# Kernel tuning notes

Measured on AMD Instinct MI355X. Metric: run time of the kernel, lower is better.

The kernel has to match this reference:

```python
import jax, jax.numpy as jnp
import numpy as np
from jax import lax

ALPHA = 2.0          # HausdorffDistanceLoss alpha
W_CE, W_BD, W_HD = 1.0, 0.5, 0.5   # combined-loss weights
NOSEED = 1e4         # sentinel 1D distance for lines with no seed pixel (>> max real distance)


def _sq_dt_binary(seed):
    """Exact squared 1D distance (along last axis) to nearest True pixel. seed: [..., L] bool."""
    L = seed.shape[-1]
    idx = jnp.arange(L, dtype=jnp.int32)
    left = lax.cummax(jnp.where(seed, idx, -1), axis=seed.ndim - 1)
    right = lax.cummin(jnp.where(seed, idx, 2 * L), axis=seed.ndim - 1, reverse=True)
    dl = jnp.where(left >= 0, (idx - left).astype(jnp.float32), jnp.float32(NOSEED))
    dr = jnp.where(right < 2 * L, (right - idx).astype(jnp.float32), jnp.float32(NOSEED))
    d = jnp.minimum(dl, dr)
    return d * d


def _sq_dt_general(f):
    """d[j] = min_y f[..., y] + (j - y)^2 along last axis (lower envelope, brute force via scan)."""
    L = f.shape[-1]
    idx = jnp.arange(L, dtype=f.dtype)
    fm = jnp.moveaxis(f, -1, 0)  # [L, ...]
    def step(carry, inp):
        fy, y = inp
        cand = fy[..., None] + (idx - y) ** 2  # [..., L]
        return jnp.minimum(carry, cand), None
    init = jnp.full(f.shape, jnp.float32(1e18), f.dtype)
    d, _ = lax.scan(step, init, (fm, idx))
    return d


def edt(seed):
    """Exact 2D Euclidean distance to nearest True pixel. seed: [..., H, W] bool.
    Equivalent to scipy.ndimage.distance_transform_edt(~seed)... i.e. scipy's
    distance_transform_edt(m) == edt(m == 0)."""
    g = jnp.swapaxes(_sq_dt_binary(jnp.swapaxes(seed, -1, -2)), -1, -2)  # pass along H
    return jnp.sqrt(_sq_dt_general(g))  # pass along W


def setup_inputs() -> dict:
    key = jax.random.key(0)
    k1, k2 = jax.random.split(key)
    pred = jax.random.normal(k1, (8, 4, 256, 256), dtype=jnp.float32)
    target = jax.random.randint(k2, (8, 256, 256), 0, 4).astype(jnp.int64)
    return {"pred": pred, "target": target}


def reference(pred, target):
    N, C, H, W = pred.shape
    tgt = target.astype(jnp.int32)

    # --- CrossEntropyLoss (mean over N,H,W) ---
    log_p = jax.nn.log_softmax(pred, axis=1)
    ce = -jnp.mean(jnp.take_along_axis(log_p, tgt[:, None, :, :], axis=1))

    p = jnp.exp(log_p)  # softmax probabilities

    # one-hot target as bool mask [N, C, H, W]
    m = tgt[:, None, :, :] == jnp.arange(C, dtype=jnp.int32)[None, :, None, None]

    # signed distance map: distance_transform_edt(~m) - distance_transform_edt(m)
    dist_to_fg = edt(m)    # == scipy distance_transform_edt(~m): dist to nearest foreground
    dist_to_bg = edt(~m)   # == scipy distance_transform_edt(m):  dist to nearest background
    signed_dm = dist_to_fg - dist_to_bg  # negative inside object

    # --- BoundaryLoss (exclude background channel 0) ---
    bd = jnp.mean(jnp.sum(p[:, 1:] * signed_dm[:, 1:], axis=(2, 3)))

    # --- HausdorffDistanceLoss (exclude background) ---
    dt_gt = dist_to_fg[:, 1:]                     # distance_transform_edt(gt_mask == 0)
    pred_seed = lax.stop_gradient(p[:, 1:]) >= 0.5  # threshold is detached in torch code
    dt_pred = edt(pred_seed)                      # distance_transform_edt(pred < 0.5)
    gt_f = m[:, 1:].astype(p.dtype)
    term1 = jnp.mean(p[:, 1:] * dt_gt ** ALPHA, axis=(2, 3))   # per (n, c) spatial means
    term2 = jnp.mean(gt_f * dt_pred ** ALPHA, axis=(2, 3))
    hd = (jnp.sum(term1) + jnp.sum(term2)) / (2 * N * (C - 1))

    total = W_CE * ce + W_BD * bd + W_HD * hd
    return total, ce, bd, hd
```

## Files before the change

kernel.cpp:

```cpp
#include <hip/hip_runtime.h>

#define NB 8
#define NC 4
#define HH 256
#define WW 256
#define HW_ (HH * WW)
#define NSL 24
#define CT 8
#define NT (WW/CT)
#define HP (HH + 1)

typedef unsigned long long u64;

__global__ __launch_bounds__(256) void k_softmax_ce(
    const float* __restrict__ pred, const int* __restrict__ tgt,
    float* __restrict__ pbuf, u64* __restrict__ rmT, u64* __restrict__ rmP,
    double* __restrict__ pce) {
  int b = blockIdx.x;
  int n = b >> 8, h = b & (HH - 1);
  int w = threadIdx.x;
  size_t base = (size_t)n * NC * HW_ + (size_t)h * WW + w;
  float x0 = pred[base];
  float x1 = pred[base + HW_];
  float x2 = pred[base + 2 * HW_];
  float x3 = pred[base + 3 * HW_];
  float mx = fmaxf(fmaxf(x0, x1), fmaxf(x2, x3));
  float e0 = __expf(x0 - mx), e1 = __expf(x1 - mx);
  float e2 = __expf(x2 - mx), e3 = __expf(x3 - mx);
  float sum = e0 + e1 + e2 + e3;
  float lse = mx + __logf(sum);
  int t = tgt[(size_t)n * HW_ + h * WW + w];
  float xt = (t == 0) ? x0 : (t == 1) ? x1 : (t == 2) ? x2 : x3;
  float ce = lse - xt;
  float inv = 1.0f / sum;
  float p1 = e1 * inv, p2 = e2 * inv, p3 = e3 * inv;
  size_t pb = ((size_t)(n * 3)) * HW_ + (size_t)h * WW + w;
  pbuf[pb]           = p1;
  pbuf[pb + HW_]     = p2;
  pbuf[pb + 2 * HW_] = p3;
  u64 bT1 = __ballot(t == 1), bP1 = __ballot(p1 >= 0.5f);
  u64 bT2 = __ballot(t == 2), bP2 = __ballot(p2 >= 0.5f);
  u64 bT3 = __ballot(t == 3), bP3 = __ballot(p3 >= 0.5f);
  int v = threadIdx.x >> 6;
  if ((threadIdx.x & 63) == 0) {
    size_t mi = ((size_t)(n * 3) * HH + h) * 4 + v;
    rmT[mi]                      = bT1;  rmP[mi]                      = bP1;
    rmT[mi + (size_t)HH * 4]     = bT2;  rmP[mi + (size_t)HH * 4]     = bP2;
    rmT[mi + (size_t)2 * HH * 4] = bT3;  rmP[mi + (size_t)2 * HH * 4] = bP3;
  }
  double cd = (double)ce;
  #pragma unroll
  for (int o = 32; o > 0; o >>= 1) cd += __shfl_down(cd, o, 64);
  if ((threadIdx.x & 63) == 0) pce[(b << 2) | v] = cd;
}

template<int WORD>
__device__ __forceinline__ int nsb_left(u64 m0, u64 m1, u64 m2, u64 m3, int bit) {
  u64 cur = (WORD == 0) ? m0 : (WORD == 1) ? m1 : (WORD == 2) ? m2 : m3;
  u64 below = cur & ((bit == 63) ? ~0ull : ((1ull << (bit + 1)) - 1ull));
  if (below) return bit - (63 - (int)__builtin_clzll(below));
  if constexpr (WORD >= 1) {
    u64 x = (WORD == 1) ? m0 : (WORD == 2) ? m1 : m2;
    if (x) return bit + 1 + (int)__builtin_clzll(x);
  }
  if constexpr (WORD >= 2) {
    u64 x = (WORD == 2) ? m0 : m1;
    if (x) return bit + 65 + (int)__builtin_clzll(x);
  }
  if constexpr (WORD >= 3) {
    if (m0) return bit + 129 + (int)__builtin_clzll(m0);
  }
  return 10000;
}

template<int WORD>
__device__ __forceinline__ int nsb_right(u64 m0, u64 m1, u64 m2, u64 m3, int bit) {
  u64 cur = (WORD == 0) ? m0 : (WORD == 1) ? m1 : (WORD == 2) ? m2 : m3;
  u64 above = cur & (~0ull << bit);
  if (above) return (int)__builtin_ctzll(above) - bit;
  if constexpr (WORD <= 2) {
    u64 x = (WORD == 0) ? m1 : (WORD == 1) ? m2 : m3;
    if (x) return 64 + (int)__builtin_ctzll(x) - bit;
  }
  if constexpr (WORD <= 1) {
    u64 x = (WORD == 0) ? m2 : m3;
    if (x) return 128 + (int)__builtin_ctzll(x) - bit;
  }
  if constexpr (WORD == 0) {
    if (m3) return 192 + (int)__builtin_ctzll(m3) - bit;
  }
  return 10000;
}

template<int WORD>
__device__ __forceinline__ void filltile(
    u64 t0, u64 t1, u64 t2, u64 t3, u64 p0, u64 p1, u64 p2, u64 p3,
    int h, int bit0, float gF[CT][HP], float gB[CT][HP], float gQ[CT][HP],
    unsigned char gtb[CT][HH + 4]) {
  u64 b0 = ~t0, b1 = ~t1, b2 = ~t2, b3 = ~t3;
  u64 curT = (WORD == 0) ? t0 : (WORD == 1) ? t1 : (WORD == 2) ? t2 : t3;
  u64 curP = (WORD == 0) ? p0 : (WORD == 1) ? p1 : (WORD == 2) ? p2 : p3;
  int dF[CT], dB[CT], dQ[CT];
  int lF = nsb_left<WORD>(t0, t1, t2, t3, bit0);
  int lB = nsb_left<WORD>(b0, b1, b2, b3, bit0);
  int lP = nsb_left<WORD>(p0, p1, p2, p3, bit0);
  #pragma unroll
  for (int wi = 0; wi < CT; ++wi) {
    int bit = bit0 + wi;
    int sF = (int)((curT >> bit) & 1ull);
    int sP = (int)((curP >> bit) & 1ull);
    if (wi > 0) {
      lF = sF ? 0 : min(lF + 1, 10000);
      lB = sF ? min(lB + 1, 10000) : 0;
      lP = sP ? 0 : min(lP + 1, 10000);
    }
    dF[wi] = lF; dB[wi] = lB; dQ[wi] = lP;
  }
  int rF = nsb_right<WORD>(t0, t1, t2, t3, bit0 + CT - 1);
  int rB = nsb_right<WORD>(b0, b1, b2, b3, bit0 + CT - 1);
  int rP = nsb_right<WORD>(p0, p1, p2, p3, bit0 + CT - 1);
  #pragma unroll
  for (int wi = CT - 1; wi >= 0; --wi) {
    int bit = bit0 + wi;
    int sF = (int)((curT >> bit) & 1ull);
    int sP = (int)((curP >> bit) & 1ull);
    if (wi < CT - 1) {
      rF = sF ? 0 : min(rF + 1, 10000);
      rB = sF ? min(rB + 1, 10000) : 0;
      rP = sP ? 0 : min(rP + 1, 10000);
    }
    int vF = min(dF[wi], rF), vB = min(dB[wi], rB), vQ = min(dQ[wi], rP);
    gF[wi][h] = (float)(vF * vF);
    gB[wi][h] = (float)(vB * vB);
    gQ[wi][h] = (float)(vQ * vQ);
    gtb[wi][h] = (unsigned char)sF;
  }
}

__global__ __launch_bounds__(256) void k_env(
    const u64* __restrict__ rmT, const u64* __restrict__ rmP,
    const float* __restrict__ pbuf, double* __restrict__ part) {
  __shared__ float gF[CT][HP];
  __shared__ float gB[CT][HP];
  __shared__ float gQ[CT][HP];
  __shared__ float pp[CT][HP];
  __shared__ unsigned char gtb[CT][HH + 4];
  __shared__ double sbuf[12];
  int s  = blockIdx.x;
  int w0 = blockIdx.y * CT;
  int h  = threadIdx.x;
  {
    size_t mi = ((size_t)s * HH + h) * 4;
    const ulonglong2* pT = (const ulonglong2*)(rmT + mi);
    const ulonglong2* pP = (const ulonglong2*)(rmP + mi);
    ulonglong2 a0 = pT[0], a1 = pT[1];
    ulonglong2 c0 = pP[0], c1 = pP[1];
    const float* prow = pbuf + (size_t)s * HW_ + (size_t)h * WW + w0;
    float4 pa = *(const float4*)prow;
    float4 pc = *(const float4*)(prow + 4);
    pp[0][h] = pa.x; pp[1][h] = pa.y; pp[2][h] = pa.z; pp[3][h] = pa.w;
    pp[4][h] = pc.x; pp[5][h] = pc.y; pp[6][h] = pc.z; pp[7][h] = pc.w;
    int bit0 = w0 & 63;
    switch (w0 >> 6) {
      case 0: filltile<0>(a0.x,a0.y,a1.x,a1.y,c0.x,c0.y,c1.x,c1.y,h,bit0,gF,gB,gQ,gtb); break;
      case 1: filltile<1>(a0.x,a0.y,a1.x,a1.y,c0.x,c0.y,c1.x,c1.y,h,bit0,gF,gB,gQ,gtb); break;
      case 2: filltile<2>(a0.x,a0.y,a1.x,a1.y,c0.x,c0.y,c1.x,c1.y,h,bit0,gF,gB,gQ,gtb); break;
      default: filltile<3>(a0.x,a0.y,a1.x,a1.y,c0.x,c0.y,c1.x,c1.y,h,bit0,gF,gB,gQ,gtb); break;
    }
  }
  __syncthreads();
  int wi = threadIdx.x & (CT - 1);
  int hg = threadIdx.x >> 3;
  double a_bd = 0.0, a_t1 = 0.0, a_t2 = 0.0;
  for (int k = 0; k < 8; ++k) {
    int h2 = hg * 8 + k;
    float mF = gF[wi][h2], mB = gB[wi][h2], mQ = gQ[wi][h2];
    for (int r = 1; r < HH; ++r) {
      float rr = (float)(r * r);
      if (rr >= mF) break;
      int u = h2 - r, d = h2 + r;
      if (u >= 0) mF = fminf(mF, gF[wi][u] + rr);
      if (d < HH) mF = fminf(mF, gF[wi][d] + rr);
    }
    for (int r = 1; r < HH; ++r) {
      float rr = (float)(r * r);
      if (rr >= mB) break;
      int u = h2 - r, d = h2 + r;
      if (u >= 0) mB = fminf(mB, gB[wi][u] + rr);
      if (d < HH) mB = fminf(mB, gB[wi][d] + rr);
    }
    for (int r = 1; r < HH; ++r) {
      float rr = (float)(r * r);
      if (rr >= mQ) break;
      int u = h2 - r, d = h2 + r;
      if (u >= 0) mQ = fminf(mQ, gQ[wi][u] + rr);
      if (d < HH) mQ = fminf(mQ, gQ[wi][d] + rr);
    }
    float dfg = sqrtf(mF), dbg = sqrtf(mB), dpr = sqrtf(mQ);
    float p  = pp[wi][h2];
    float gt = (float)gtb[wi][h2];
    a_bd += (double)(p * (dfg - dbg));
    a_t1 += (double)(p * dfg * dfg);
    a_t2 += (double)(gt * dpr * dpr);
  }
  int lane = threadIdx.x & 63, wid = threadIdx.x >> 6;
  #pragma unroll
  for (int o = 32; o > 0; o >>= 1) {
    a_bd += __shfl_down(a_bd, o, 64);
    a_t1 += __shfl_down(a_t1, o, 64);
    a_t2 += __shfl_down(a_t2, o, 64);
  }
  if (lane == 0) { sbuf[wid*3] = a_bd; sbuf[wid*3+1] = a_t1; sbuf[wid*3+2] = a_t2; }
  __syncthreads();
  if (threadIdx.x == 0) {
    double b = 0, t1 = 0, t2 = 0;
    #pragma unroll
    for (int i = 0; i < 4; ++i) { b += sbuf[i*3]; t1 += sbuf[i*3+1]; t2 += sbuf[i*3+2]; }
    size_t pi = ((size_t)s * NT + blockIdx.y) * 4;
    part[pi] = b; part[pi+1] = t1; part[pi+2] = t2;
  }
}

__global__ __launch_bounds__(256) void k_final(const double* __restrict__ pce,
    const double* __restrict__ part, float* __restrict__ out) {
  __shared__ double sb[16];
  int t = threadIdx.x;
  double ce = 0.0, bd = 0.0, t1 = 0.0, t2 = 0.0;
  for (int i = t; i < NB * HH * 4; i += 256) ce += pce[i];
  for (int i = t; i < NSL * NT; i += 256) {
    bd += part[(size_t)i * 4];
    t1 += part[(size_t)i * 4 + 1];
    t2 += part[(size_t)i * 4 + 2];
  }
  int lane = t & 63, wid = t >> 6;
  #pragma unroll
  for (int o = 32; o > 0; o >>= 1) {
    ce += __shfl_down(ce, o, 64);
    bd += __shfl_down(bd, o, 64);
    t1 += __shfl_down(t1, o, 64);
    t2 += __shfl_down(t2, o, 64);
  }
  if (lane == 0) { sb[wid*4]=ce; sb[wid*4+1]=bd; sb[wid*4+2]=t1; sb[wid*4+3]=t2; }
  __syncthreads();
  if (t == 0) {
    double c = 0, b = 0, u1 = 0, u2 = 0;
    #pragma unroll
    for (int i = 0; i < 4; ++i) { c += sb[i*4]; b += sb[i*4+1]; u1 += sb[i*4+2]; u2 += sb[i*4+3]; }
    c /= (double)(NB * HW_);
    b /= (double)NSL;
    double hd = (u1 + u2) / ((double)HW_ * (double)(2 * NB * (NC - 1)));
    out[0] = (float)(c + 0.5 * b + 0.5 * hd);
    out[1] = (float)c;
    out[2] = (float)b;
    out[3] = (float)hd;
  }
}

extern "C" void kernel_launch(void* const* d_in, const int* in_sizes, int n_in,
                              void* d_out, int out_size, void* d_ws, size_t ws_size,
                              hipStream_t stream) {
  (void)in_sizes; (void)n_in; (void)out_size; (void)ws_size;
  const float* pred = (const float*)d_in[0];
  const int*   tgt  = (const int*)d_in[1];
  float* out = (float*)d_out;
  char* ws = (char*)d_ws;
  double* pce  = (double*)ws;
  double* part = (double*)(ws + 65536);
  float*  pbuf = (float*)(ws + 131072);
  u64* rmT = (u64*)(ws + 131072 + (size_t)NSL * HW_ * 4);
  u64* rmP = rmT + (size_t)NSL * HH * 4;

  hipLaunchKernelGGL(k_softmax_ce, dim3(NB * HH), dim3(256), 0, stream,
                     pred, tgt, pbuf, rmT, rmP, pce);
  hipLaunchKernelGGL(k_env, dim3(NSL, NT), dim3(256), 0, stream,
                     rmT, rmP, pbuf, part);
  hipLaunchKernelGGL(k_final, dim3(1), dim3(256), 0, stream, pce, part, out);
}
```

Before: 91.74 us.

## Fuse softmax, envelope and final reduction into one cooperative kernel

Merges the three kernels into a single cooperative launch of 768 blocks, separated by grid-wide syncs. Each block grid-strides over the softmax/CE rows, then does its envelope tile, and block 0 does the final reduction. The aim is to remove two kernel launch gaps and the tail of each launch. In exchange the launch needs all 768 blocks co-resident and adds grid-sync overhead. The CE phase now runs at lower parallelism per block, with 2048 rows spread over 768 blocks.

```diff
diff --git a/kernel.cpp b/kernel.cpp
--- a/kernel.cpp
+++ b/kernel.cpp
@@ -1,4 +1,7 @@
 #include <hip/hip_runtime.h>
+#include <hip/hip_cooperative_groups.h>
+
+namespace cg = cooperative_groups;
 
 #define NB 8
 #define NC 4
@@ -9,50 +12,9 @@
 #define CT 8
 #define NT (WW/CT)
 #define HP (HH + 1)
+#define GRIDN (NSL * NT)
 
 typedef unsigned long long u64;
-
-__global__ __launch_bounds__(256) void k_softmax_ce(
-    const float* __restrict__ pred, const int* __restrict__ tgt,
-    float* __restrict__ pbuf, u64* __restrict__ rmT, u64* __restrict__ rmP,
-    double* __restrict__ pce) {
-  int b = blockIdx.x;
-  int n = b >> 8, h = b & (HH - 1);
-  int w = threadIdx.x;
-  size_t base = (size_t)n * NC * HW_ + (size_t)h * WW + w;
-  float x0 = pred[base];
-  float x1 = pred[base + HW_];
-  float x2 = pred[base + 2 * HW_];
-  float x3 = pred[base + 3 * HW_];
-  float mx = fmaxf(fmaxf(x0, x1), fmaxf(x2, x3));
-  float e0 = __expf(x0 - mx), e1 = __expf(x1 - mx);
-  float e2 = __expf(x2 - mx), e3 = __expf(x3 - mx);
-  float sum = e0 + e1 + e2 + e3;
-  float lse = mx + __logf(sum);
-  int t = tgt[(size_t)n * HW_ + h * WW + w];
-  float xt = (t == 0) ? x0 : (t == 1) ? x1 : (t == 2) ? x2 : x3;
-  float ce = lse - xt;
-  float inv = 1.0f / sum;
-  float p1 = e1 * inv, p2 = e2 * inv, p3 = e3 * inv;
-  size_t pb = ((size_t)(n * 3)) * HW_ + (size_t)h * WW + w;
-  pbuf[pb]           = p1;
-  pbuf[pb + HW_]     = p2;
-  pbuf[pb + 2 * HW_] = p3;
-  u64 bT1 = __ballot(t == 1), bP1 = __ballot(p1 >= 0.5f);
-  u64 bT2 = __ballot(t == 2), bP2 = __ballot(p2 >= 0.5f);
-  u64 bT3 = __ballot(t == 3), bP3 = __ballot(p3 >= 0.5f);
-  int v = threadIdx.x >> 6;
-  if ((threadIdx.x & 63) == 0) {
-    size_t mi = ((size_t)(n * 3) * HH + h) * 4 + v;
-    rmT[mi]                      = bT1;  rmP[mi]                      = bP1;
-    rmT[mi + (size_t)HH * 4]     = bT2;  rmP[mi + (size_t)HH * 4]     = bP2;
-    rmT[mi + (size_t)2 * HH * 4] = bT3;  rmP[mi + (size_t)2 * HH * 4] = bP3;
-  }
-  double cd = (double)ce;
-  #pragma unroll
-  for (int o = 32; o > 0; o >>= 1) cd += __shfl_down(cd, o, 64);
-  if ((threadIdx.x & 63) == 0) pce[(b << 2) | v] = cd;
-}
 
 template<int WORD>
 __device__ __forceinline__ int nsb_left(u64 m0, u64 m1, u64 m2, u64 m3, int bit) {
@@ -137,122 +99,176 @@
   }
 }
 
-__global__ __launch_bounds__(256) void k_env(
-    const u64* __restrict__ rmT, const u64* __restrict__ rmP,
-    const float* __restrict__ pbuf, double* __restrict__ part) {
+__global__ __launch_bounds__(256) void k_fused(
+    const float* __restrict__ pred, const int* __restrict__ tgt,
+    float* __restrict__ pbuf, u64* __restrict__ rmT, u64* __restrict__ rmP,
+    double* __restrict__ pce, double* __restrict__ part,
+    float* __restrict__ out) {
   __shared__ float gF[CT][HP];
   __shared__ float gB[CT][HP];
   __shared__ float gQ[CT][HP];
   __shared__ float pp[CT][HP];
   __shared__ unsigned char gtb[CT][HH + 4];
-  __shared__ double sbuf[12];
-  int s  = blockIdx.x;
-  int w0 = blockIdx.y * CT;
-  int h  = threadIdx.x;
+  __shared__ double sbuf[16];
+  cg::grid_group grid = cg::this_grid();
+  int tid = threadIdx.x;
+  int lane = tid & 63, wid = tid >> 6;
+
   {
-    size_t mi = ((size_t)s * HH + h) * 4;
-    const ulonglong2* pT = (const ulonglong2*)(rmT + mi);
-    const ulonglong2* pP = (const ulonglong2*)(rmP + mi);
-    ulonglong2 a0 = pT[0], a1 = pT[1];
-    ulonglong2 c0 = pP[0], c1 = pP[1];
-    const float* prow = pbuf + (size_t)s * HW_ + (size_t)h * WW + w0;
-    float4 pa = *(const float4*)prow;
-    float4 pc = *(const float4*)(prow + 4);
-    pp[0][h] = pa.x; pp[1][h] = pa.y; pp[2][h] = pa.z; pp[3][h] = pa.w;
-    pp[4][h] = pc.x; pp[5][h] = pc.y; pp[6][h] = pc.z; pp[7][h] = pc.w;
-    int bit0 = w0 & 63;
-    switch (w0 >> 6) {
-      case 0: filltile<0>(a0.x,a0.y,a1.x,a1.y,c0.x,c0.y,c1.x,c1.y,h,bit0,gF,gB,gQ,gtb); break;
-      case 1: filltile<1>(a0.x,a0.y,a1.x,a1.y,c0.x,c0.y,c1.x,c1.y,h,bit0,gF,gB,gQ,gtb); break;
-      case 2: filltile<2>(a0.x,a0.y,a1.x,a1.y,c0.x,c0.y,c1.x,c1.y,h,bit0,gF,gB,gQ,gtb); break;
-      default: filltile<3>(a0.x,a0.y,a1.x,a1.y,c0.x,c0.y,c1.x,c1.y,h,bit0,gF,gB,gQ,gtb); break;
-    }
-  }
-  __syncthreads();
-  int wi = threadIdx.x & (CT - 1);
-  int hg = threadIdx.x >> 3;
-  double a_bd = 0.0, a_t1 = 0.0, a_t2 = 0.0;
-  for (int k = 0; k < 8; ++k) {
-    int h2 = hg * 8 + k;
-    float mF = gF[wi][h2], mB = gB[wi][h2], mQ = gQ[wi][h2];
-    for (int r = 1; r < HH; ++r) {
-      float rr = (float)(r * r);
-      if (rr >= mF) break;
-      int u = h2 - r, d = h2 + r;
-      if (u >= 0) mF = fminf(mF, gF[wi][u] + rr);
-      if (d < HH) mF = fminf(mF, gF[wi][d] + rr);
-    }
-    for (int r = 1; r < HH; ++r) {
-      float rr = (float)(r * r);
-      if (rr >= mB) break;
-      int u = h2 - r, d = h2 + r;
-      if (u >= 0) mB = fminf(mB, gB[wi][u] + rr);
-      if (d < HH) mB = fminf(mB, gB[wi][d] + rr);
-    }
-    for (int r = 1; r < HH; ++r) {
-      float rr = (float)(r * r);
-      if (rr >= mQ) break;
-      int u = h2 - r, d = h2 + r;
-      if (u >= 0) mQ = fminf(mQ, gQ[wi][u] + rr);
-      if (d < HH) mQ = fminf(mQ, gQ[wi][d] + rr);
-    }
-    float dfg = sqrtf(mF), dbg = sqrtf(mB), dpr = sqrtf(mQ);
-    float p  = pp[wi][h2];
-    float gt = (float)gtb[wi][h2];
-    a_bd += (double)(p * (dfg - dbg));
-    a_t1 += (double)(p * dfg * dfg);
-    a_t2 += (double)(gt * dpr * dpr);
-  }
-  int lane = threadIdx.x & 63, wid = threadIdx.x >> 6;
-  #pragma unroll
-  for (int o = 32; o > 0; o >>= 1) {
-    a_bd += __shfl_down(a_bd, o, 64);
-    a_t1 += __shfl_down(a_t1, o, 64);
-    a_t2 += __shfl_down(a_t2, o, 64);
-  }
-  if (lane == 0) { sbuf[wid*3] = a_bd; sbuf[wid*3+1] = a_t1; sbuf[wid*3+2] = a_t2; }
-  __syncthreads();
-  if (threadIdx.x == 0) {
-    double b = 0, t1 = 0, t2 = 0;
+    double ced = 0.0;
+    int w = tid;
+    for (int b = blockIdx.x; b < NB * HH; b += GRIDN) {
+      int n = b >> 8, h = b & (HH - 1);
+      size_t base = (size_t)n * NC * HW_ + (size_t)h * WW + w;
+      float x0 = pred[base];
+      float x1 = pred[base + HW_];
+      float x2 = pred[base + 2 * HW_];
+      float x3 = pred[base + 3 * HW_];
+      float mx = fmaxf(fmaxf(x0, x1), fmaxf(x2, x3));
+      float e0 = __expf(x0 - mx), e1 = __expf(x1 - mx);
+      float e2 = __expf(x2 - mx), e3 = __expf(x3 - mx);
+      float sum = e0 + e1 + e2 + e3;
+      float lse = mx + __logf(sum);
+      int t = tgt[(size_t)n * HW_ + h * WW + w];
+      float xt = (t == 0) ? x0 : (t == 1) ? x1 : (t == 2) ? x2 : x3;
+      ced += (double)(lse - xt);
+      float inv = 1.0f / sum;
+      float p1 = e1 * inv, p2 = e2 * inv, p3 = e3 * inv;
+      size_t pb = ((size_t)(n * 3)) * HW_ + (size_t)h * WW + w;
+      pbuf[pb]           = p1;
+      pbuf[pb + HW_]     = p2;
+      pbuf[pb + 2 * HW_] = p3;
+      u64 bT1 = __ballot(t == 1), bP1 = __ballot(p1 >= 0.5f);
+      u64 bT2 = __ballot(t == 2), bP2 = __ballot(p2 >= 0.5f);
+      u64 bT3 = __ballot(t == 3), bP3 = __ballot(p3 >= 0.5f);
+      if (lane == 0) {
+        size_t mi = ((size_t)(n * 3) * HH + h) * 4 + wid;
+        rmT[mi]                      = bT1;  rmP[mi]                      = bP1;
+        rmT[mi + (size_t)HH * 4]     = bT2;  rmP[mi + (size_t)HH * 4]     = bP2;
+        rmT[mi + (size_t)2 * HH * 4] = bT3;  rmP[mi + (size_t)2 * HH * 4] = bP3;
+      }
+    }
     #pragma unroll
-    for (int i = 0; i < 4; ++i) { b += sbuf[i*3]; t1 += sbuf[i*3+1]; t2 += sbuf[i*3+2]; }
-    size_t pi = ((size_t)s * NT + blockIdx.y) * 4;
-    part[pi] = b; part[pi+1] = t1; part[pi+2] = t2;
-  }
-}
-
-__global__ __launch_bounds__(256) void k_final(const double* __restrict__ pce,
-    const double* __restrict__ part, float* __restrict__ out) {
-  __shared__ double sb[16];
-  int t = threadIdx.x;
-  double ce = 0.0, bd = 0.0, t1 = 0.0, t2 = 0.0;
-  for (int i = t; i < NB * HH * 4; i += 256) ce += pce[i];
-  for (int i = t; i < NSL * NT; i += 256) {
-    bd += part[(size_t)i * 4];
-    t1 += part[(size_t)i * 4 + 1];
-    t2 += part[(size_t)i * 4 + 2];
-  }
-  int lane = t & 63, wid = t >> 6;
-  #pragma unroll
-  for (int o = 32; o > 0; o >>= 1) {
-    ce += __shfl_down(ce, o, 64);
-    bd += __shfl_down(bd, o, 64);
-    t1 += __shfl_down(t1, o, 64);
-    t2 += __shfl_down(t2, o, 64);
-  }
-  if (lane == 0) { sb[wid*4]=ce; sb[wid*4+1]=bd; sb[wid*4+2]=t1; sb[wid*4+3]=t2; }
-  __syncthreads();
-  if (t == 0) {
-    double c = 0, b = 0, u1 = 0, u2 = 0;
+    for (int o = 32; o > 0; o >>= 1) ced += __shfl_down(ced, o, 64);
+    if (lane == 0) sbuf[wid] = ced;
+    __syncthreads();
+    if (tid == 0) {
+      double r = sbuf[0] + sbuf[1] + sbuf[2] + sbuf[3];
+      pce[blockIdx.x] = r;
+    }
+    __syncthreads();
+  }
+  __threadfence();
+  grid.sync();
+
+  {
+    int s  = blockIdx.x >> 5;
+    int w0 = (blockIdx.x & 31) * CT;
+    int h  = tid;
+    {
+      size_t mi = ((size_t)s * HH + h) * 4;
+      const ulonglong2* pT = (const ulonglong2*)(rmT + mi);
+      const ulonglong2* pP = (const ulonglong2*)(rmP + mi);
+      ulonglong2 a0 = pT[0], a1 = pT[1];
+      ulonglong2 c0 = pP[0], c1 = pP[1];
+      const float* prow = pbuf + (size_t)s * HW_ + (size_t)h * WW + w0;
+      float4 pa = *(const float4*)prow;
+      float4 pc = *(const float4*)(prow + 4);
+      pp[0][h] = pa.x; pp[1][h] = pa.y; pp[2][h] = pa.z; pp[3][h] = pa.w;
+      pp[4][h] = pc.x; pp[5][h] = pc.y; pp[6][h] = pc.z; pp[7][h] = pc.w;
+      int bit0 = w0 & 63;
+      switch (w0 >> 6) {
+        case 0: filltile<0>(a0.x,a0.y,a1.x,a1.y,c0.x,c0.y,c1.x,c1.y,h,bit0,gF,gB,gQ,gtb); break;
+        case 1: filltile<1>(a0.x,a0.y,a1.x,a1.y,c0.x,c0.y,c1.x,c1.y,h,bit0,gF,gB,gQ,gtb); break;
+        case 2: filltile<2>(a0.x,a0.y,a1.x,a1.y,c0.x,c0.y,c1.x,c1.y,h,bit0,gF,gB,gQ,gtb); break;
+        default: filltile<3>(a0.x,a0.y,a1.x,a1.y,c0.x,c0.y,c1.x,c1.y,h,bit0,gF,gB,gQ,gtb); break;
+      }
+    }
+    __syncthreads();
+    int wi = tid & (CT - 1);
+    int hg = tid >> 3;
+    double a_bd = 0.0, a_t1 = 0.0, a_t2 = 0.0;
+    for (int k = 0; k < 8; ++k) {
+      int h2 = hg * 8 + k;
+      float mF = gF[wi][h2], mB = gB[wi][h2], mQ = gQ[wi][h2];
+      for (int r = 1; r < HH; ++r) {
+        float rr = (float)(r * r);
+        if (rr >= mF) break;
+        int u = h2 - r, d = h2 + r;
+        if (u >= 0) mF = fminf(mF, gF[wi][u] + rr);
+        if (d < HH) mF = fminf(mF, gF[wi][d] + rr);
+      }
+      for (int r = 1; r < HH; ++r) {
+        float rr = (float)(r * r);
+        if (rr >= mB) break;
+        int u = h2 - r, d = h2 + r;
+        if (u >= 0) mB = fminf(mB, gB[wi][u] + rr);
+        if (d < HH) mB = fminf(mB, gB[wi][d] + rr);
+      }
+      for (int r = 1; r < HH; ++r) {
+        float rr = (float)(r * r);
+        if (rr >= mQ) break;
+        int u = h2 - r, d = h2 + r;
+        if (u >= 0) mQ = fminf(mQ, gQ[wi][u] + rr);
+        if (d < HH) mQ = fminf(mQ, gQ[wi][d] + rr);
+      }
+      float dfg = sqrtf(mF), dbg = sqrtf(mB), dpr = sqrtf(mQ);
+      float p  = pp[wi][h2];
+      float gt = (float)gtb[wi][h2];
+      a_bd += (double)(p * (dfg - dbg));
+      a_t1 += (double)(p * dfg * dfg);
+      a_t2 += (double)(gt * dpr * dpr);
+    }
     #pragma unroll
-    for (int i = 0; i < 4; ++i) { c += sb[i*4]; b += sb[i*4+1]; u1 += sb[i*4+2]; u2 += sb[i*4+3]; }
-    c /= (double)(NB * HW_);
-    b /= (double)NSL;
-    double hd = (u1 + u2) / ((double)HW_ * (double)(2 * NB * (NC - 1)));
-    out[0] = (float)(c + 0.5 * b + 0.5 * hd);
-    out[1] = (float)c;
-    out[2] = (float)b;
-    out[3] = (float)hd;
+    for (int o = 32; o > 0; o >>= 1) {
+      a_bd += __shfl_down(a_bd, o, 64);
+      a_t1 += __shfl_down(a_t1, o, 64);
+      a_t2 += __shfl_down(a_t2, o, 64);
+    }
+    __syncthreads();
+    if (lane == 0) { sbuf[wid*3] = a_bd; sbuf[wid*3+1] = a_t1; sbuf[wid*3+2] = a_t2; }
+    __syncthreads();
+    if (tid == 0) {
+      double b = 0, t1 = 0, t2 = 0;
+      #pragma unroll
+      for (int i = 0; i < 4; ++i) { b += sbuf[i*3]; t1 += sbuf[i*3+1]; t2 += sbuf[i*3+2]; }
+      size_t pi = (size_t)blockIdx.x * 4;
+      part[pi] = b; part[pi+1] = t1; part[pi+2] = t2;
+    }
+  }
+  __threadfence();
+  grid.sync();
+
+  if (blockIdx.x == 0) {
+    double ce = 0.0, bd = 0.0, t1 = 0.0, t2 = 0.0;
+    for (int i = tid; i < GRIDN; i += 256) {
+      ce += pce[i];
+      bd += part[(size_t)i * 4];
+      t1 += part[(size_t)i * 4 + 1];
+      t2 += part[(size_t)i * 4 + 2];
+    }
+    #pragma unroll
+    for (int o = 32; o > 0; o >>= 1) {
+      ce += __shfl_down(ce, o, 64);
+      bd += __shfl_down(bd, o, 64);
+      t1 += __shfl_down(t1, o, 64);
+      t2 += __shfl_down(t2, o, 64);
+    }
+    __syncthreads();
+    if (lane == 0) { sbuf[wid*4]=ce; sbuf[wid*4+1]=bd; sbuf[wid*4+2]=t1; sbuf[wid*4+3]=t2; }
+    __syncthreads();
+    if (tid == 0) {
+      double c = 0, b = 0, u1 = 0, u2 = 0;
+      #pragma unroll
+      for (int i = 0; i < 4; ++i) { c += sbuf[i*4]; b += sbuf[i*4+1]; u1 += sbuf[i*4+2]; u2 += sbuf[i*4+3]; }
+      c /= (double)(NB * HW_);
+      b /= (double)NSL;
+      double hd = (u1 + u2) / ((double)HW_ * (double)(2 * NB * (NC - 1)));
+      out[0] = (float)(c + 0.5 * b + 0.5 * hd);
+      out[1] = (float)c;
+      out[2] = (float)b;
+      out[3] = (float)hd;
+    }
   }
 }
 
@@ -265,14 +281,13 @@
   float* out = (float*)d_out;
   char* ws = (char*)d_ws;
   double* pce  = (double*)ws;
-  double* part = (double*)(ws + 65536);
-  float*  pbuf = (float*)(ws + 131072);
-  u64* rmT = (u64*)(ws + 131072 + (size_t)NSL * HW_ * 4);
+  double* part = (double*)(ws + 8192);
+  float*  pbuf = (float*)(ws + 65536);
+  u64* rmT = (u64*)(ws + 65536 + (size_t)NSL * HW_ * 4);
   u64* rmP = rmT + (size_t)NSL * HH * 4;
 
-  hipLaunchKernelGGL(k_softmax_ce, dim3(NB * HH), dim3(256), 0, stream,
-                     pred, tgt, pbuf, rmT, rmP, pce);
-  hipLaunchKernelGGL(k_env, dim3(NSL, NT), dim3(256), 0, stream,
-                     rmT, rmP, pbuf, part);
-  hipLaunchKernelGGL(k_final, dim3(1), dim3(256), 0, stream, pce, part, out);
-}
+  void* args[] = {(void*)&pred, (void*)&tgt, (void*)&pbuf, (void*)&rmT,
+                  (void*)&rmP, (void*)&pce, (void*)&part, (void*)&out};
+  hipLaunchCooperativeKernel((const void*)k_fused, dim3(GRIDN), dim3(256),
+                             args, 0, stream);
+}
```

New measurement: 302.1 us. 3.29x slower.
